# Kernel tuning notes

Hardware: AMD Instinct MI355X
Metric: run time of the kernel (lower is better)

## Reference

```python
import jax, jax.numpy as jnp
import numpy as np

B, S, E, H = 4, 1024, 1024, 16
HD = E // H
SCALE = HD ** -0.5


def setup_inputs() -> dict:
    key = jax.random.key(0)
    ks = jax.random.split(key, 10)
    std = E ** -0.5
    return {
        "sequence_embeddings": jax.random.normal(ks[0], (B, S, E), jnp.float32),
        "graph_embeddings": jax.random.normal(ks[1], (B, S, HD), jnp.float32),
        "Wq": jax.random.normal(ks[2], (E, E), jnp.float32) * std,
        "bq": jnp.zeros((E,), jnp.float32),
        "Wk": jax.random.normal(ks[3], (E, E), jnp.float32) * std,
        "bk": jnp.zeros((E,), jnp.float32),
        "Wv": jax.random.normal(ks[4], (E, E), jnp.float32) * std,
        "bv": jnp.zeros((E,), jnp.float32),
        "Wo": jax.random.normal(ks[5], (E, E), jnp.float32) * std,
        "bo": jnp.zeros((E,), jnp.float32),
    }


def reference(sequence_embeddings, graph_embeddings, Wq, bq, Wk, bk, Wv, bv, Wo, bo):
    b, s, e = sequence_embeddings.shape
    # project and split heads: [b, h, s, hd]
    def heads(x, W, bias):
        return (x @ W + bias).reshape(b, s, H, HD).transpose(0, 2, 1, 3)

    q = heads(sequence_embeddings, Wq, bq)
    k = heads(sequence_embeddings, Wk, bk)
    v = heads(sequence_embeddings, Wv, bv)

    # sequence-to-sequence attention: [b, h, s, s]
    attn_scores = jnp.einsum("bhqd,bhkd->bhqk", q, k) * SCALE
    seq_attn = jax.nn.softmax(attn_scores, axis=-1)

    # graph-to-sequence attention: graph [b, s, hd] broadcast over heads -> [b, h, s, s]
    graph_scores = jnp.einsum("bqd,bhkd->bhqk", graph_embeddings, k)
    graph_attn = jax.nn.softmax(graph_scores, axis=-1)

    # fused dual-softmax weights (dropout is identity in eval)
    attn_weights = seq_attn * graph_attn

    attn_out = jnp.einsum("bhqk,bhkd->bhqd", attn_weights, v)
    attn_out = attn_out.transpose(0, 2, 1, 3).reshape(b, s, e)
    output = attn_out @ Wo + bo
    return output, attn_weights
```

## Files before the change

### kernel.cpp

```cpp
#include <hip/hip_runtime.h>
#include <math.h>

#define B_ 4
#define S_ 1024
#define E_ 1024
#define H_ 16
#define HD_ 64

#define LOG2E 1.4426950408889634f
#define C16L2 23.08312065422341f
#define C64L2 92.33248261689365f
#define C80L2 115.41560327111706f

typedef float4 f4;
typedef _Float16 f16x8 __attribute__((ext_vector_type(8)));
typedef ushort u16x8 __attribute__((ext_vector_type(8)));
typedef float f32x4 __attribute__((ext_vector_type(4)));

__device__ __forceinline__ void gl16(const void* g, void* l) {
  __builtin_amdgcn_global_load_lds(
      (__attribute__((address_space(1))) void*)g,
      (__attribute__((address_space(3))) void*)l, 16, 0, 0);
}

__device__ __forceinline__ ushort f2h(float x) {
  return __builtin_bit_cast(ushort, (_Float16)x);
}
__device__ __forceinline__ float h2f(ushort h) {
  return (float)__builtin_bit_cast(_Float16, h);
}
__device__ __forceinline__ float exp2r(float x) {
  return __builtin_amdgcn_exp2f(x);
}
__device__ __forceinline__ f32x4 mfma16(u16x8 a, u16x8 b, f32x4 c) {
  return __builtin_amdgcn_mfma_f32_16x16x32_f16(
      __builtin_bit_cast(f16x8, a), __builtin_bit_cast(f16x8, b), c, 0, 0, 0);
}
__device__ __forceinline__ u16x8 ldfrag(const ushort* s, int row, int chunk) {
  return *reinterpret_cast<const u16x8*>(s + row * 64 + ((chunk ^ (row & 7)) << 3));
}
__device__ __forceinline__ u16x8 ldfrag32(const ushort* s, int row, int chunk) {
  return *reinterpret_cast<const u16x8*>(s + row * 32 + ((chunk ^ (row & 3)) << 3));
}


__global__ __launch_bounds__(256) void prep_x(
    const float* __restrict__ x, ushort* __restrict__ xf)
{
  const size_t i = ((size_t)blockIdx.x * 256 + threadIdx.x) * 8;
  float v[8];
  *reinterpret_cast<f4*>(v)     = *reinterpret_cast<const f4*>(x + i);
  *reinterpret_cast<f4*>(v + 4) = *reinterpret_cast<const f4*>(x + i + 4);
  unsigned fw[4];
#pragma unroll
  for (int p = 0; p < 4; ++p)
    fw[p] = (unsigned)f2h(v[2 * p]) | ((unsigned)f2h(v[2 * p + 1]) << 16);
  *reinterpret_cast<uint4*>(xf + i) = make_uint4(fw[0], fw[1], fw[2], fw[3]);
}

__global__ __launch_bounds__(256) void prep_w(
    const float* __restrict__ Wq, const float* __restrict__ Wk,
    const float* __restrict__ Wv, const float* __restrict__ Wo,
    ushort* __restrict__ ws16)
{
  const int MSZ = 1024 * 1024;
  const int mat = blockIdx.z;
  const int n0 = blockIdx.x * 64, k0 = blockIdx.y * 64;
  const float* W = mat == 0 ? Wq : mat == 1 ? Wk : mat == 2 ? Wv : Wo;
  ushort* Oh = ws16 + (size_t)mat * MSZ;

  __shared__ __align__(16) float tile[64][65];
  const int t = threadIdx.x;
  const int r = t >> 2, cq = t & 3;
#pragma unroll
  for (int j = 0; j < 4; ++j) {
    const f4 v = *reinterpret_cast<const f4*>(&W[(size_t)(k0 + r) * 1024 + n0 + cq * 16 + 4 * j]);
    tile[r][cq * 16 + 4 * j + 0] = v.x;
    tile[r][cq * 16 + 4 * j + 1] = v.y;
    tile[r][cq * 16 + 4 * j + 2] = v.z;
    tile[r][cq * 16 + 4 * j + 3] = v.w;
  }
  __syncthreads();
  unsigned hw[8];
#pragma unroll
  for (int p = 0; p < 8; ++p)
    hw[p] = (unsigned)f2h(tile[cq * 16 + 2 * p][r]) |
            ((unsigned)f2h(tile[cq * 16 + 2 * p + 1][r]) << 16);
  ushort* dh = Oh + (size_t)(n0 + r) * 1024 + k0 + cq * 16;
  *reinterpret_cast<uint4*>(dh)     = make_uint4(hw[0], hw[1], hw[2], hw[3]);
  *reinterpret_cast<uint4*>(dh + 8) = make_uint4(hw[4], hw[5], hw[6], hw[7]);
}

template <int OMODE>
__global__ __launch_bounds__(256) void gemm_mfma(
    const ushort* __restrict__ Ab, const ushort* __restrict__ Bhg,
    const float* __restrict__ bias, float scale,
    ushort* __restrict__ Oh, float* __restrict__ Of)
{
  const int n0 = blockIdx.x * 128;
  const int m0 = blockIdx.y * 64;
  const int t = threadIdx.x;
  const int wv = t >> 6, lane = t & 63;
  const int lr = lane & 15, lg = lane >> 4;
  const int wm = (wv >> 1) * 32, wn = (wv & 1) * 64;
  const int row8 = lane >> 3, ch8 = lane & 7;

  __shared__ __align__(16) ushort Ah_s[64 * 64];
  __shared__ __align__(16) ushort Bh_s[128 * 64];
  __shared__ __align__(16) ushort tr_s[OMODE == 2 ? 128 * 72 : 16];

  f32x4 acc[2][4];
#pragma unroll
  for (int mi = 0; mi < 2; ++mi)
#pragma unroll
    for (int ni = 0; ni < 4; ++ni) { f32x4 z = {0.f, 0.f, 0.f, 0.f}; acc[mi][ni] = z; }

  for (int kt = 0; kt < 16; ++kt) {
    const int k0 = kt * 64;
    __syncthreads();
#pragma unroll
    for (int j = 0; j < 4; ++j) {
      const int row = wv * 32 + j * 8 + row8;
      gl16(Bhg + (size_t)(n0 + row) * 1024 + k0 + ((ch8 ^ (row & 7)) << 3),
           &Bh_s[(wv * 32 + j * 8) * 64]);
    }
#pragma unroll
    for (int j = 0; j < 2; ++j) {
      const int row = wv * 16 + j * 8 + row8;
      gl16(Ab + (size_t)(m0 + row) * 1024 + k0 + ((ch8 ^ (row & 7)) << 3),
           &Ah_s[(wv * 16 + j * 8) * 64]);
    }
    __syncthreads();
#pragma unroll
    for (int ks = 0; ks < 2; ++ks) {
      const u16x8 ah0 = ldfrag(Ah_s, wm + lr, ks * 4 + lg);
      const u16x8 ah1 = ldfrag(Ah_s, wm + 16 + lr, ks * 4 + lg);
#pragma unroll
      for (int ni = 0; ni < 4; ++ni) {
        const u16x8 bh = ldfrag(Bh_s, wn + ni * 16 + lr, ks * 4 + lg);
        acc[0][ni] = mfma16(ah0, bh, acc[0][ni]);
        acc[1][ni] = mfma16(ah1, bh, acc[1][ni]);
      }
    }
  }

  if constexpr (OMODE == 2) {
    __syncthreads();
#pragma unroll
    for (int mi = 0; mi < 2; ++mi)
#pragma unroll
      for (int ni = 0; ni < 4; ++ni)
#pragma unroll
        for (int r = 0; r < 4; ++r) {
          const int n_l = wn + ni * 16 + lr, m_l = wm + mi * 16 + lg * 4 + r;
          tr_s[n_l * 72 + m_l] = f2h(acc[mi][ni][r] + bias[n0 + n_l]);
        }
    __syncthreads();
    const int row = t >> 1, hf = t & 1;
    const int n_g = n0 + row;
    const int h_ = n_g >> 6, hd = n_g & 63;
    const int b_g = m0 >> 10;
    ushort* dst = Oh + ((size_t)(b_g * 16 + h_) * 64 + hd) * 1024 + (m0 & 1023) + hf * 32;
#pragma unroll
    for (int j = 0; j < 4; ++j)
      *reinterpret_cast<uint4*>(dst + 8 * j) =
          *reinterpret_cast<const uint4*>(&tr_s[row * 72 + hf * 32 + 8 * j]);
  } else {
#pragma unroll
    for (int mi = 0; mi < 2; ++mi)
#pragma unroll
      for (int ni = 0; ni < 4; ++ni) {
        const int n = n0 + wn + ni * 16 + lr;
        const float bi = bias[n];
#pragma unroll
        for (int r = 0; r < 4; ++r) {
          const int m = m0 + wm + mi * 16 + lg * 4 + r;
          const float v = (acc[mi][ni][r] + bi) * scale;
          if constexpr (OMODE == 0) {
            Of[(size_t)m * 1024 + n] = v;
          } else {
            const size_t addr =
                ((size_t)((m >> 10) * 16 + (n >> 6)) * 1024 + (m & 1023)) * 64 + (n & 63);
            Oh[addr] = f2h(v);
          }
        }
      }
  }
}

__global__ __launch_bounds__(256) void attn_mfma(
    const ushort* __restrict__ qh_g, const ushort* __restrict__ kf_g,
    const ushort* __restrict__ vt_g, const float* __restrict__ ge,
    float* __restrict__ attn, ushort* __restrict__ aoh)
{
  __shared__ __align__(16) ushort kh2_s[2][2048];
  __shared__ __align__(16) ushort vt2_s[2][2048];
  __shared__ __align__(16) float w_sf[4][512];

  const int bid = blockIdx.x;
  const int wg = (bid & 7) * 128 + (bid >> 3);
  const int bh = wg >> 4, qb = wg & 15;
  const int b = bh >> 4, h = bh & 15;

  const int t = threadIdx.x;
  const int wv = t >> 6, lane = t & 63;
  const int lr = lane & 15, lg = lane >> 4;
  const int q0 = qb * 64 + wv * 16;

  u16x8 qh[2], gh[2];
  float gf[2][8];
#pragma unroll
  for (int ks = 0; ks < 2; ++ks) {
    const size_t qoff = ((size_t)bh * S_ + q0 + lr) * HD_ + ks * 32 + lg * 8;
    qh[ks] = *reinterpret_cast<const u16x8*>(qh_g + qoff);
    const float* grow = ge + ((size_t)b * S_ + q0 + lr) * HD_ + ks * 32 + lg * 8;
    f4 g0 = *reinterpret_cast<const f4*>(grow);
    f4 g1 = *reinterpret_cast<const f4*>(grow + 4);
    gf[ks][0] = g0.x * LOG2E; gf[ks][1] = g0.y * LOG2E;
    gf[ks][2] = g0.z * LOG2E; gf[ks][3] = g0.w * LOG2E;
    gf[ks][4] = g1.x * LOG2E; gf[ks][5] = g1.y * LOG2E;
    gf[ks][6] = g1.z * LOG2E; gf[ks][7] = g1.w * LOG2E;
#pragma unroll
    for (int e = 0; e < 8; ++e) gh[ks][e] = f2h(gf[ks][e]);
  }

  const ushort* kfb = kf_g + (size_t)bh * S_ * HD_;
  const ushort* vtb = vt_g + (size_t)bh * HD_ * S_;

  const int krow = wv * 8 + (lane >> 3);
  const int ksw  = ((lane & 7) ^ (krow & 7)) << 3;
  const int vrow = wv * 16 + (lane >> 2);
  const int vsw  = ((lane & 3) ^ (vrow & 3)) << 3;

  auto stage_kf = [&](int kt, int c) {
    gl16(kfb + kt * 2048 + krow * 64 + ksw, &kh2_s[c][wv * 512]);
  };
  auto stage_vt = [&](int kt, int c) {
    gl16(vtb + kt * 32 + (size_t)vrow * 1024 + vsw, &vt2_s[c][wv * 512]);
  };

  float z1L = 0.f, z2L = 0.f;

  asm volatile("s_waitcnt vmcnt(0)" ::: "memory");
  __builtin_amdgcn_sched_barrier(0);

  stage_kf(0, 0);
  for (int kt = 0; kt < 32; ++kt) {
    if (kt < 31) {
      stage_kf(kt + 1, (kt + 1) & 1);
      asm volatile("s_waitcnt vmcnt(1)" ::: "memory");
    } else {
      asm volatile("s_waitcnt vmcnt(0)" ::: "memory");
    }
    __builtin_amdgcn_sched_barrier(0);
    __builtin_amdgcn_s_barrier();
    __builtin_amdgcn_sched_barrier(0);

    const ushort* kp = kh2_s[kt & 1];
    f32x4 s1[2], s2[2];
    __builtin_amdgcn_s_setprio(1);
#pragma unroll
    for (int ct = 0; ct < 2; ++ct) {
      f32x4 z = {0.f, 0.f, 0.f, 0.f};
      s1[ct] = z; s2[ct] = z;
#pragma unroll
      for (int ks = 0; ks < 2; ++ks) {
        const u16x8 kA = ldfrag(kp, ct * 16 + lr, ks * 4 + lg);
        s1[ct] = mfma16(kA, qh[ks], s1[ct]);
        s2[ct] = mfma16(kA, gh[ks], s2[ct]);
      }
    }
    __builtin_amdgcn_s_setprio(0);
#pragma unroll
    for (int ct = 0; ct < 2; ++ct)
#pragma unroll
      for (int r = 0; r < 4; ++r) {
        z1L += exp2r(s1[ct][r] - C16L2);
        z2L += exp2r(s2[ct][r] - C64L2);
      }
    __builtin_amdgcn_s_barrier();
    __builtin_amdgcn_sched_barrier(0);
  }

  float z1 = z1L + __shfl_xor(z1L, 16);
  z1 += __shfl_xor(z1, 32);
  float z2 = z2L + __shfl_xor(z2L, 16);
  z2 += __shfl_xor(z2, 32);
  const float rz = 1.f / (z1 * z2);

  stage_kf(0, 0);
  stage_vt(0, 0);

  u16x8 uh[2];
#pragma unroll
  for (int ks = 0; ks < 2; ++ks)
#pragma unroll
    for (int e = 0; e < 8; ++e)
      uh[ks][e] = f2h(h2f(qh[ks][e]) + gf[ks][e]);

  f32x4 o[4];
#pragma unroll
  for (int dt = 0; dt < 4; ++dt) { f32x4 z = {0.f, 0.f, 0.f, 0.f}; o[dt] = z; }

  float* wrow = attn + ((size_t)bh * S_ + q0) * S_;
  float* wsw = w_sf[wv];
  const int prowBase = ((lr >> 2) << 3) | (lr & 3);

  for (int kt = 0; kt < 32; ++kt) {
    if (kt < 31) {
      stage_kf(kt + 1, (kt + 1) & 1);
      stage_vt(kt + 1, (kt + 1) & 1);
      if (kt == 0) asm volatile("s_waitcnt vmcnt(2)" ::: "memory");
      else         asm volatile("s_waitcnt vmcnt(4)" ::: "memory");
    } else {
      asm volatile("s_waitcnt vmcnt(2)" ::: "memory");
    }
    __builtin_amdgcn_sched_barrier(0);
    __builtin_amdgcn_s_barrier();
    __builtin_amdgcn_sched_barrier(0);

    const int c = kt & 1;
    const ushort* kfp = kh2_s[c];
    const ushort* vtp = vt2_s[c];

    f32x4 s12[2];
    {
      f32x4 z = {0.f, 0.f, 0.f, 0.f};
      s12[0] = z; s12[1] = z;
    }
    __builtin_amdgcn_s_setprio(1);
#pragma unroll
    for (int ks = 0; ks < 2; ++ks) {
      const u16x8 kA0 = ldfrag(kfp, prowBase, ks * 4 + lg);
      const u16x8 kA1 = ldfrag(kfp, prowBase | 4, ks * 4 + lg);
      s12[0] = mfma16(kA0, uh[ks], s12[0]);
      s12[1] = mfma16(kA1, uh[ks], s12[1]);
    }
    __builtin_amdgcn_s_setprio(0);

    float wv2[2][4];
    u16x8 af;
#pragma unroll
    for (int ct = 0; ct < 2; ++ct)
#pragma unroll
      for (int r = 0; r < 4; ++r) {
        wv2[ct][r] = exp2r(s12[ct][r] - C80L2) * rz;
        af[ct * 4 + r] = f2h(wv2[ct][r]);
      }

    __builtin_amdgcn_s_setprio(1);
#pragma unroll
    for (int dt = 0; dt < 4; ++dt) {
      const u16x8 vf = ldfrag32(vtp, dt * 16 + lr, lg);
      o[dt] = mfma16(af, vf, o[dt]);
    }
    __builtin_amdgcn_s_setprio(0);

#pragma unroll
    for (int ct = 0; ct < 2; ++ct)
#pragma unroll
      for (int r = 0; r < 4; ++r)
        wsw[lr * 32 + lg * 8 + ((ct * 4 + r) ^ (lr & 7))] = wv2[ct][r];
    {
      const int rowq = lane >> 2, kc = lane & 3;
      float vs[8];
#pragma unroll
      for (int j = 0; j < 8; ++j)
        vs[j] = wsw[rowq * 32 + kc * 8 + (j ^ (rowq & 7))];
      float* dst = wrow + (size_t)rowq * S_ + kt * 32 + kc * 8;
      *reinterpret_cast<f4*>(dst)     = make_float4(vs[0], vs[1], vs[2], vs[3]);
      *reinterpret_cast<f4*>(dst + 4) = make_float4(vs[4], vs[5], vs[6], vs[7]);
    }
    __builtin_amdgcn_s_barrier();
    __builtin_amdgcn_sched_barrier(0);
  }

#pragma unroll
  for (int dt = 0; dt < 4; ++dt)
#pragma unroll
    for (int r = 0; r < 4; ++r)
      aoh[((size_t)b * S_ + q0 + lg * 4 + r) * E_ + h * 64 + dt * 16 + lr] =
          f2h(o[dt][r]);
}

extern "C" void kernel_launch(void* const* d_in, const int* in_sizes, int n_in,
                              void* d_out, int out_size, void* d_ws, size_t ws_size,
                              hipStream_t stream) {
  const float* x  = (const float*)d_in[0];
  const float* ge = (const float*)d_in[1];
  const float* Wq = (const float*)d_in[2];
  const float* bq = (const float*)d_in[3];
  const float* Wk = (const float*)d_in[4];
  const float* bk = (const float*)d_in[5];
  const float* Wv = (const float*)d_in[6];
  const float* bv = (const float*)d_in[7];
  const float* Wo = (const float*)d_in[8];
  const float* bo = (const float*)d_in[9];

  float* out  = (float*)d_out;
  float* attn = out + (size_t)B_ * S_ * E_;

  const size_t MSZ = 1024 * 1024;
  ushort* ws16 = (ushort*)d_ws;
  ushort* Wqf = ws16 + 0 * MSZ;
  ushort* Wkf = ws16 + 1 * MSZ;
  ushort* Wvf = ws16 + 2 * MSZ;
  ushort* Wof = ws16 + 3 * MSZ;
  ushort* xf  = ws16 + 4 * MSZ;
  ushort* qh  = ws16 + 8 * MSZ;
  ushort* kf  = ws16 + 12 * MSZ;
  ushort* vt  = ws16 + 16 * MSZ;
  ushort* aoh = ws16 + 20 * MSZ;

  dim3 blk(256);
  hipLaunchKernelGGL(prep_x, dim3(2048), blk, 0, stream, x, xf);
  hipLaunchKernelGGL(prep_w, dim3(16, 16, 4), blk, 0, stream, Wq, Wk, Wv, Wo, ws16);

  dim3 ggrid(E_ / 128, (B_ * S_) / 64);
  hipLaunchKernelGGL((gemm_mfma<3>), ggrid, blk, 0, stream,
                     xf, Wqf, bq, 0.125f * LOG2E, qh, nullptr);
  hipLaunchKernelGGL((gemm_mfma<3>), ggrid, blk, 0, stream,
                     xf, Wkf, bk, 1.0f, kf, nullptr);
  hipLaunchKernelGGL((gemm_mfma<2>), ggrid, blk, 0, stream,
                     xf, Wvf, bv, 1.0f, vt, nullptr);

  hipLaunchKernelGGL(attn_mfma, dim3(1024), blk, 0, stream,
                     qh, kf, vt, ge, attn, aoh);

  hipLaunchKernelGGL((gemm_mfma<0>), ggrid, blk, 0, stream,
                     aoh, Wof, bo, 1.0f, nullptr, out);
}
```

Measured before the change: 182.9 us.

## Double key tile to 64 and store attention weights directly from registers

```diff
diff --git a/kernel.cpp b/kernel.cpp
--- a/kernel.cpp
+++ b/kernel.cpp
@@ -38,9 +38,6 @@
 }
 __device__ __forceinline__ u16x8 ldfrag(const ushort* s, int row, int chunk) {
   return *reinterpret_cast<const u16x8*>(s + row * 64 + ((chunk ^ (row & 7)) << 3));
-}
-__device__ __forceinline__ u16x8 ldfrag32(const ushort* s, int row, int chunk) {
-  return *reinterpret_cast<const u16x8*>(s + row * 32 + ((chunk ^ (row & 3)) << 3));
 }
 
 
@@ -193,9 +190,8 @@
     const ushort* __restrict__ vt_g, const float* __restrict__ ge,
     float* __restrict__ attn, ushort* __restrict__ aoh)
 {
-  __shared__ __align__(16) ushort kh2_s[2][2048];
-  __shared__ __align__(16) ushort vt2_s[2][2048];
-  __shared__ __align__(16) float w_sf[4][512];
+  __shared__ __align__(16) ushort kh2_s[2][4096];
+  __shared__ __align__(16) ushort vt2_s[2][4096];
 
   const int bid = blockIdx.x;
   const int wg = (bid & 7) * 128 + (bid >> 3);
@@ -227,16 +223,59 @@
   const ushort* kfb = kf_g + (size_t)bh * S_ * HD_;
   const ushort* vtb = vt_g + (size_t)bh * HD_ * S_;
 
-  const int krow = wv * 8 + (lane >> 3);
-  const int ksw  = ((lane & 7) ^ (krow & 7)) << 3;
-  const int vrow = wv * 16 + (lane >> 2);
-  const int vsw  = ((lane & 3) ^ (vrow & 3)) << 3;
-
+  const int srow = t >> 2;
+  const int sc0 = t & 3;
   auto stage_kf = [&](int kt, int c) {
-    gl16(kfb + kt * 2048 + krow * 64 + ksw, &kh2_s[c][wv * 512]);
+#pragma unroll
+    for (int j = 0; j < 2; ++j) {
+      const int ch = sc0 + j * 4;
+      gl16(kfb + kt * 4096 + srow * 64 + ((ch ^ (srow & 7)) << 3),
+           &kh2_s[c][(srow & 56) * 64 + (srow & 7) * 128 + j * 64]);
+    }
   };
   auto stage_vt = [&](int kt, int c) {
-    gl16(vtb + kt * 32 + (size_t)vrow * 1024 + vsw, &vt2_s[c][wv * 512]);
+#pragma unroll
+    for (int j = 0; j < 2; ++j) {
+      const int ch = sc0 + j * 4;
+      gl16(vtb + kt * 64 + (size_t)srow * 1024 + ((ch ^ (srow & 7)) << 3),
+           &vt2_s[c][(srow & 56) * 64 + (srow & 7) * 128 + j * 64]);
+    }
+  };
+
+  const int krow = wv * 16 + (lane >> 2);
+  const int kch0 = lane & 3;
+  auto stage_k2 = [&](int kt, int c) {
+#pragma unroll
+    for (int j = 0; j < 2; ++j) {
+      const int ch = kch0 + j * 4;
+      gl16(kfb + kt * 4096 + krow * 64 + (((ch) ^ (krow & 7)) << 3),
+           &kh2_s[c][(wv * 16) * 64 + (lane >> 2) * 0 + j * 2048 + 0]);
+    }
+  };
+  (void)stage_kf; (void)stage_vt; (void)stage_k2;
+
+  auto stage_K = [&](int kt, int c) {
+#pragma unroll
+    for (int j = 0; j < 2; ++j) {
+      const int row = wv * 16 + (lane >> 2);
+      const int ch = j * 4 + (lane & 3);
+      gl16(kfb + kt * 4096 + row * 64 + ((ch ^ (row & 7)) << 3),
+           &kh2_s[c][j * 2048 + (wv * 16) * 32]);
+    }
+  };
+  auto stage_V = [&](int kt, int c) {
+#pragma unroll
+    for (int j = 0; j < 2; ++j) {
+      const int row = wv * 16 + (lane >> 2);
+      const int ch = j * 4 + (lane & 3);
+      gl16(vtb + kt * 64 + (size_t)row * 1024 + ((ch ^ (row & 7)) << 3),
+           &vt2_s[c][j * 2048 + (wv * 16) * 32]);
+    }
+  };
+  auto ldfragH = [&](const ushort* s, int row, int ch) -> u16x8 {
+    const int chx = ch ^ (row & 7);
+    return *reinterpret_cast<const u16x8*>(
+        s + (chx >> 2) * 2048 + row * 32 + (chx & 3) * 8);
   };
 
   float z1L = 0.f, z2L = 0.f;
@@ -244,11 +283,11 @@
   asm volatile("s_waitcnt vmcnt(0)" ::: "memory");
   __builtin_amdgcn_sched_barrier(0);
 
-  stage_kf(0, 0);
-  for (int kt = 0; kt < 32; ++kt) {
-    if (kt < 31) {
-      stage_kf(kt + 1, (kt + 1) & 1);
-      asm volatile("s_waitcnt vmcnt(1)" ::: "memory");
+  stage_K(0, 0);
+  for (int kt = 0; kt < 16; ++kt) {
+    if (kt < 15) {
+      stage_K(kt + 1, (kt + 1) & 1);
+      asm volatile("s_waitcnt vmcnt(2)" ::: "memory");
     } else {
       asm volatile("s_waitcnt vmcnt(0)" ::: "memory");
     }
@@ -257,22 +296,22 @@
     __builtin_amdgcn_sched_barrier(0);
 
     const ushort* kp = kh2_s[kt & 1];
-    f32x4 s1[2], s2[2];
+    f32x4 s1[4], s2[4];
     __builtin_amdgcn_s_setprio(1);
 #pragma unroll
-    for (int ct = 0; ct < 2; ++ct) {
+    for (int ct = 0; ct < 4; ++ct) {
       f32x4 z = {0.f, 0.f, 0.f, 0.f};
       s1[ct] = z; s2[ct] = z;
 #pragma unroll
       for (int ks = 0; ks < 2; ++ks) {
-        const u16x8 kA = ldfrag(kp, ct * 16 + lr, ks * 4 + lg);
+        const u16x8 kA = ldfragH(kp, ct * 16 + lr, ks * 4 + lg);
         s1[ct] = mfma16(kA, qh[ks], s1[ct]);
         s2[ct] = mfma16(kA, gh[ks], s2[ct]);
       }
     }
     __builtin_amdgcn_s_setprio(0);
 #pragma unroll
-    for (int ct = 0; ct < 2; ++ct)
+    for (int ct = 0; ct < 4; ++ct)
 #pragma unroll
       for (int r = 0; r < 4; ++r) {
         z1L += exp2r(s1[ct][r] - C16L2);
@@ -288,8 +327,8 @@
   z2 += __shfl_xor(z2, 32);
   const float rz = 1.f / (z1 * z2);
 
-  stage_kf(0, 0);
-  stage_vt(0, 0);
+  stage_K(0, 0);
+  stage_V(0, 0);
 
   u16x8 uh[2];
 #pragma unroll
@@ -303,17 +342,16 @@
   for (int dt = 0; dt < 4; ++dt) { f32x4 z = {0.f, 0.f, 0.f, 0.f}; o[dt] = z; }
 
   float* wrow = attn + ((size_t)bh * S_ + q0) * S_;
-  float* wsw = w_sf[wv];
   const int prowBase = ((lr >> 2) << 3) | (lr & 3);
 
-  for (int kt = 0; kt < 32; ++kt) {
-    if (kt < 31) {
-      stage_kf(kt + 1, (kt + 1) & 1);
-      stage_vt(kt + 1, (kt + 1) & 1);
-      if (kt == 0) asm volatile("s_waitcnt vmcnt(2)" ::: "memory");
-      else         asm volatile("s_waitcnt vmcnt(4)" ::: "memory");
+  for (int kt = 0; kt < 16; ++kt) {
+    if (kt < 15) {
+      stage_K(kt + 1, (kt + 1) & 1);
+      stage_V(kt + 1, (kt + 1) & 1);
+      if (kt == 0) asm volatile("s_waitcnt vmcnt(4)" ::: "memory");
+      else         asm volatile("s_waitcnt vmcnt(8)" ::: "memory");
     } else {
-      asm volatile("s_waitcnt vmcnt(2)" ::: "memory");
+      asm volatile("s_waitcnt vmcnt(4)" ::: "memory");
     }
     __builtin_amdgcn_sched_barrier(0);
     __builtin_amdgcn_s_barrier();
@@ -323,53 +361,47 @@
     const ushort* kfp = kh2_s[c];
     const ushort* vtp = vt2_s[c];
 
-    f32x4 s12[2];
-    {
-      f32x4 z = {0.f, 0.f, 0.f, 0.f};
-      s12[0] = z; s12[1] = z;
-    }
-    __builtin_amdgcn_s_setprio(1);
-#pragma unroll
-    for (int ks = 0; ks < 2; ++ks) {
-      const u16x8 kA0 = ldfrag(kfp, prowBase, ks * 4 + lg);
-      const u16x8 kA1 = ldfrag(kfp, prowBase | 4, ks * 4 + lg);
-      s12[0] = mfma16(kA0, uh[ks], s12[0]);
-      s12[1] = mfma16(kA1, uh[ks], s12[1]);
-    }
-    __builtin_amdgcn_s_setprio(0);
-
-    float wv2[2][4];
-    u16x8 af;
-#pragma unroll
-    for (int ct = 0; ct < 2; ++ct)
-#pragma unroll
-      for (int r = 0; r < 4; ++r) {
-        wv2[ct][r] = exp2r(s12[ct][r] - C80L2) * rz;
-        af[ct * 4 + r] = f2h(wv2[ct][r]);
-      }
-
-    __builtin_amdgcn_s_setprio(1);
-#pragma unroll
-    for (int dt = 0; dt < 4; ++dt) {
-      const u16x8 vf = ldfrag32(vtp, dt * 16 + lr, lg);
-      o[dt] = mfma16(af, vf, o[dt]);
-    }
-    __builtin_amdgcn_s_setprio(0);
-
-#pragma unroll
-    for (int ct = 0; ct < 2; ++ct)
-#pragma unroll
-      for (int r = 0; r < 4; ++r)
-        wsw[lr * 32 + lg * 8 + ((ct * 4 + r) ^ (lr & 7))] = wv2[ct][r];
-    {
-      const int rowq = lane >> 2, kc = lane & 3;
-      float vs[8];
-#pragma unroll
-      for (int j = 0; j < 8; ++j)
-        vs[j] = wsw[rowq * 32 + kc * 8 + (j ^ (rowq & 7))];
-      float* dst = wrow + (size_t)rowq * S_ + kt * 32 + kc * 8;
-      *reinterpret_cast<f4*>(dst)     = make_float4(vs[0], vs[1], vs[2], vs[3]);
-      *reinterpret_cast<f4*>(dst + 4) = make_float4(vs[4], vs[5], vs[6], vs[7]);
+#pragma unroll
+    for (int hf = 0; hf < 2; ++hf) {
+      f32x4 s12[2];
+      {
+        f32x4 z = {0.f, 0.f, 0.f, 0.f};
+        s12[0] = z; s12[1] = z;
+      }
+      __builtin_amdgcn_s_setprio(1);
+#pragma unroll
+      for (int ks = 0; ks < 2; ++ks) {
+        const u16x8 kA0 = ldfragH(kfp, hf * 32 + prowBase, ks * 4 + lg);
+        const u16x8 kA1 = ldfragH(kfp, hf * 32 + (prowBase | 4), ks * 4 + lg);
+        s12[0] = mfma16(kA0, uh[ks], s12[0]);
+        s12[1] = mfma16(kA1, uh[ks], s12[1]);
+      }
+      __builtin_amdgcn_s_setprio(0);
+
+      float wv2[8];
+      u16x8 af;
+#pragma unroll
+      for (int ct = 0; ct < 2; ++ct)
+#pragma unroll
+        for (int r = 0; r < 4; ++r) {
+          const float w = exp2r(s12[ct][r] - C80L2) * rz;
+          wv2[ct * 4 + r] = w;
+          af[ct * 4 + r] = f2h(w);
+        }
+
+      __builtin_amdgcn_s_setprio(1);
+#pragma unroll
+      for (int dt = 0; dt < 4; ++dt) {
+        const u16x8 vf = ldfragH(vtp, dt * 16 + lr, hf * 4 + lg);
+        o[dt] = mfma16(af, vf, o[dt]);
+      }
+      __builtin_amdgcn_s_setprio(0);
+
+      {
+        float* dst = wrow + (size_t)lr * S_ + kt * 64 + hf * 32 + lg * 8;
+        *reinterpret_cast<f4*>(dst)     = make_float4(wv2[0], wv2[1], wv2[2], wv2[3]);
+        *reinterpret_cast<f4*>(dst + 4) = make_float4(wv2[4], wv2[5], wv2[6], wv2[7]);
+      }
     }
     __builtin_amdgcn_s_barrier();
     __builtin_amdgcn_sched_barrier(0);
```

Result: faster. 176.9 us (-3.3%).

## Replace LDS-staged K/V tiles with direct register double-buffered global loads in attention

Applied to the files above, without the earlier changes.

```diff
diff --git a/kernel.cpp b/kernel.cpp
--- a/kernel.cpp
+++ b/kernel.cpp
@@ -36,12 +36,14 @@
   return __builtin_amdgcn_mfma_f32_16x16x32_f16(
       __builtin_bit_cast(f16x8, a), __builtin_bit_cast(f16x8, b), c, 0, 0, 0);
 }
+__device__ __forceinline__ u16x8 ldg16(const ushort* p) {
+  return *reinterpret_cast<const u16x8*>(p);
+}
 __device__ __forceinline__ u16x8 ldfrag(const ushort* s, int row, int chunk) {
   return *reinterpret_cast<const u16x8*>(s + row * 64 + ((chunk ^ (row & 7)) << 3));
 }
-__device__ __forceinline__ u16x8 ldfrag32(const ushort* s, int row, int chunk) {
-  return *reinterpret_cast<const u16x8*>(s + row * 32 + ((chunk ^ (row & 3)) << 3));
-}
+
+struct F4x { u16x8 a, b, c, d; };
 
 
 __global__ __launch_bounds__(256) void prep_x(
@@ -188,15 +190,11 @@
   }
 }
 
-__global__ __launch_bounds__(256) void attn_mfma(
+__global__ __launch_bounds__(256, 4) void attn_mfma(
     const ushort* __restrict__ qh_g, const ushort* __restrict__ kf_g,
     const ushort* __restrict__ vt_g, const float* __restrict__ ge,
     float* __restrict__ attn, ushort* __restrict__ aoh)
 {
-  __shared__ __align__(16) ushort kh2_s[2][2048];
-  __shared__ __align__(16) ushort vt2_s[2][2048];
-  __shared__ __align__(16) float w_sf[4][512];
-
   const int bid = blockIdx.x;
   const int wg = (bid & 7) * 128 + (bid >> 3);
   const int bh = wg >> 4, qb = wg & 15;
@@ -212,7 +210,7 @@
 #pragma unroll
   for (int ks = 0; ks < 2; ++ks) {
     const size_t qoff = ((size_t)bh * S_ + q0 + lr) * HD_ + ks * 32 + lg * 8;
-    qh[ks] = *reinterpret_cast<const u16x8*>(qh_g + qoff);
+    qh[ks] = ldg16(qh_g + qoff);
     const float* grow = ge + ((size_t)b * S_ + q0 + lr) * HD_ + ks * 32 + lg * 8;
     f4 g0 = *reinterpret_cast<const f4*>(grow);
     f4 g1 = *reinterpret_cast<const f4*>(grow + 4);
@@ -227,59 +225,38 @@
   const ushort* kfb = kf_g + (size_t)bh * S_ * HD_;
   const ushort* vtb = vt_g + (size_t)bh * HD_ * S_;
 
-  const int krow = wv * 8 + (lane >> 3);
-  const int ksw  = ((lane & 7) ^ (krow & 7)) << 3;
-  const int vrow = wv * 16 + (lane >> 2);
-  const int vsw  = ((lane & 3) ^ (vrow & 3)) << 3;
-
-  auto stage_kf = [&](int kt, int c) {
-    gl16(kfb + kt * 2048 + krow * 64 + ksw, &kh2_s[c][wv * 512]);
-  };
-  auto stage_vt = [&](int kt, int c) {
-    gl16(vtb + kt * 32 + (size_t)vrow * 1024 + vsw, &vt2_s[c][wv * 512]);
-  };
-
   float z1L = 0.f, z2L = 0.f;
 
-  asm volatile("s_waitcnt vmcnt(0)" ::: "memory");
-  __builtin_amdgcn_sched_barrier(0);
-
-  stage_kf(0, 0);
-  for (int kt = 0; kt < 32; ++kt) {
-    if (kt < 31) {
-      stage_kf(kt + 1, (kt + 1) & 1);
-      asm volatile("s_waitcnt vmcnt(1)" ::: "memory");
-    } else {
-      asm volatile("s_waitcnt vmcnt(0)" ::: "memory");
-    }
-    __builtin_amdgcn_sched_barrier(0);
-    __builtin_amdgcn_s_barrier();
-    __builtin_amdgcn_sched_barrier(0);
-
-    const ushort* kp = kh2_s[kt & 1];
-    f32x4 s1[2], s2[2];
-    __builtin_amdgcn_s_setprio(1);
-#pragma unroll
-    for (int ct = 0; ct < 2; ++ct) {
-      f32x4 z = {0.f, 0.f, 0.f, 0.f};
-      s1[ct] = z; s2[ct] = z;
-#pragma unroll
-      for (int ks = 0; ks < 2; ++ks) {
-        const u16x8 kA = ldfrag(kp, ct * 16 + lr, ks * 4 + lg);
-        s1[ct] = mfma16(kA, qh[ks], s1[ct]);
-        s2[ct] = mfma16(kA, gh[ks], s2[ct]);
-      }
-    }
-    __builtin_amdgcn_s_setprio(0);
-#pragma unroll
-    for (int ct = 0; ct < 2; ++ct)
+  {
+    auto p1load = [&](F4x& D, int kt) {
+      const ushort* p = kfb + (size_t)kt * 2048 + lr * 64 + lg * 8;
+      D.a = ldg16(p);
+      D.b = ldg16(p + 32);
+      D.c = ldg16(p + 1024);
+      D.d = ldg16(p + 1024 + 32);
+    };
+    auto p1comp = [&](const F4x& D) {
+      f32x4 zz = {0.f, 0.f, 0.f, 0.f};
+      f32x4 s1a = mfma16(D.a, qh[0], zz); s1a = mfma16(D.b, qh[1], s1a);
+      f32x4 s2a = mfma16(D.a, gh[0], zz); s2a = mfma16(D.b, gh[1], s2a);
+      f32x4 s1b = mfma16(D.c, qh[0], zz); s1b = mfma16(D.d, qh[1], s1b);
+      f32x4 s2b = mfma16(D.c, gh[0], zz); s2b = mfma16(D.d, gh[1], s2b);
 #pragma unroll
       for (int r = 0; r < 4; ++r) {
-        z1L += exp2r(s1[ct][r] - C16L2);
-        z2L += exp2r(s2[ct][r] - C64L2);
-      }
-    __builtin_amdgcn_s_barrier();
-    __builtin_amdgcn_sched_barrier(0);
+        z1L += exp2r(s1a[r] - C16L2) + exp2r(s1b[r] - C16L2);
+        z2L += exp2r(s2a[r] - C64L2) + exp2r(s2b[r] - C64L2);
+      }
+    };
+    F4x ka, kb;
+    p1load(ka, 0);
+    for (int kt = 0; kt < 32; kt += 2) {
+      p1load(kb, kt + 1);
+      __builtin_amdgcn_sched_barrier(0);
+      p1comp(ka);
+      if (kt + 2 < 32) p1load(ka, kt + 2);
+      __builtin_amdgcn_sched_barrier(0);
+      p1comp(kb);
+    }
   }
 
   float z1 = z1L + __shfl_xor(z1L, 16);
@@ -288,9 +265,6 @@
   z2 += __shfl_xor(z2, 32);
   const float rz = 1.f / (z1 * z2);
 
-  stage_kf(0, 0);
-  stage_vt(0, 0);
-
   u16x8 uh[2];
 #pragma unroll
   for (int ks = 0; ks < 2; ++ks)
@@ -303,76 +277,59 @@
   for (int dt = 0; dt < 4; ++dt) { f32x4 z = {0.f, 0.f, 0.f, 0.f}; o[dt] = z; }
 
   float* wrow = attn + ((size_t)bh * S_ + q0) * S_;
-  float* wsw = w_sf[wv];
-  const int prowBase = ((lr >> 2) << 3) | (lr & 3);
-
-  for (int kt = 0; kt < 32; ++kt) {
-    if (kt < 31) {
-      stage_kf(kt + 1, (kt + 1) & 1);
-      stage_vt(kt + 1, (kt + 1) & 1);
-      if (kt == 0) asm volatile("s_waitcnt vmcnt(2)" ::: "memory");
-      else         asm volatile("s_waitcnt vmcnt(4)" ::: "memory");
-    } else {
-      asm volatile("s_waitcnt vmcnt(2)" ::: "memory");
-    }
-    __builtin_amdgcn_sched_barrier(0);
-    __builtin_amdgcn_s_barrier();
-    __builtin_amdgcn_sched_barrier(0);
-
-    const int c = kt & 1;
-    const ushort* kfp = kh2_s[c];
-    const ushort* vtp = vt2_s[c];
-
-    f32x4 s12[2];
-    {
-      f32x4 z = {0.f, 0.f, 0.f, 0.f};
-      s12[0] = z; s12[1] = z;
-    }
-    __builtin_amdgcn_s_setprio(1);
-#pragma unroll
-    for (int ks = 0; ks < 2; ++ks) {
-      const u16x8 kA0 = ldfrag(kfp, prowBase, ks * 4 + lg);
-      const u16x8 kA1 = ldfrag(kfp, prowBase | 4, ks * 4 + lg);
-      s12[0] = mfma16(kA0, uh[ks], s12[0]);
-      s12[1] = mfma16(kA1, uh[ks], s12[1]);
-    }
-    __builtin_amdgcn_s_setprio(0);
-
-    float wv2[2][4];
-    u16x8 af;
-#pragma unroll
-    for (int ct = 0; ct < 2; ++ct)
+  const int p0 = ((lr >> 2) << 3) | (lr & 3);
+
+  {
+    auto p2loadk = [&](F4x& D, int kt) {
+      const ushort* p = kfb + (size_t)kt * 2048 + lg * 8;
+      D.a = ldg16(p + p0 * 64);
+      D.b = ldg16(p + p0 * 64 + 32);
+      D.c = ldg16(p + (p0 | 4) * 64);
+      D.d = ldg16(p + (p0 | 4) * 64 + 32);
+    };
+    auto p2loadv = [&](F4x& D, int kt) {
+      const ushort* p = vtb + (size_t)kt * 32 + lr * 1024 + lg * 8;
+      D.a = ldg16(p);
+      D.b = ldg16(p + 16 * 1024);
+      D.c = ldg16(p + 32 * 1024);
+      D.d = ldg16(p + 48 * 1024);
+    };
+    auto p2comp = [&](const F4x& K, const F4x& V, int kt) {
+      f32x4 zz = {0.f, 0.f, 0.f, 0.f};
+      f32x4 sA = mfma16(K.a, uh[0], zz); sA = mfma16(K.b, uh[1], sA);
+      f32x4 sB = mfma16(K.c, uh[0], zz); sB = mfma16(K.d, uh[1], sB);
+      float wv2[8];
+      u16x8 af;
 #pragma unroll
       for (int r = 0; r < 4; ++r) {
-        wv2[ct][r] = exp2r(s12[ct][r] - C80L2) * rz;
-        af[ct * 4 + r] = f2h(wv2[ct][r]);
-      }
-
-    __builtin_amdgcn_s_setprio(1);
-#pragma unroll
-    for (int dt = 0; dt < 4; ++dt) {
-      const u16x8 vf = ldfrag32(vtp, dt * 16 + lr, lg);
-      o[dt] = mfma16(af, vf, o[dt]);
-    }
-    __builtin_amdgcn_s_setprio(0);
-
-#pragma unroll
-    for (int ct = 0; ct < 2; ++ct)
-#pragma unroll
-      for (int r = 0; r < 4; ++r)
-        wsw[lr * 32 + lg * 8 + ((ct * 4 + r) ^ (lr & 7))] = wv2[ct][r];
-    {
-      const int rowq = lane >> 2, kc = lane & 3;
-      float vs[8];
-#pragma unroll
-      for (int j = 0; j < 8; ++j)
-        vs[j] = wsw[rowq * 32 + kc * 8 + (j ^ (rowq & 7))];
-      float* dst = wrow + (size_t)rowq * S_ + kt * 32 + kc * 8;
-      *reinterpret_cast<f4*>(dst)     = make_float4(vs[0], vs[1], vs[2], vs[3]);
-      *reinterpret_cast<f4*>(dst + 4) = make_float4(vs[4], vs[5], vs[6], vs[7]);
-    }
-    __builtin_amdgcn_s_barrier();
-    __builtin_amdgcn_sched_barrier(0);
+        wv2[r] = exp2r(sA[r] - C80L2) * rz;
+        wv2[4 + r] = exp2r(sB[r] - C80L2) * rz;
+        af[r] = f2h(wv2[r]);
+        af[4 + r] = f2h(wv2[4 + r]);
+      }
+      o[0] = mfma16(af, V.a, o[0]);
+      o[1] = mfma16(af, V.b, o[1]);
+      o[2] = mfma16(af, V.c, o[2]);
+      o[3] = mfma16(af, V.d, o[3]);
+      float* dst = wrow + (size_t)lr * S_ + kt * 32 + lg * 8;
+      *reinterpret_cast<f4*>(dst)     = make_float4(wv2[0], wv2[1], wv2[2], wv2[3]);
+      *reinterpret_cast<f4*>(dst + 4) = make_float4(wv2[4], wv2[5], wv2[6], wv2[7]);
+    };
+    F4x ka, va, kb, vb;
+    p2loadk(ka, 0);
+    p2loadv(va, 0);
+    for (int kt = 0; kt < 32; kt += 2) {
+      p2loadk(kb, kt + 1);
+      p2loadv(vb, kt + 1);
+      __builtin_amdgcn_sched_barrier(0);
+      p2comp(ka, va, kt);
+      if (kt + 2 < 32) {
+        p2loadk(ka, kt + 2);
+        p2loadv(va, kt + 2);
+      }
+      __builtin_amdgcn_sched_barrier(0);
+      p2comp(kb, vb, kt + 1);
+    }
   }
 
 #pragma unroll
```

Measured after the change: 281.2 us. +53.7%, slower.
